# Performance work log

Measured on AMD Instinct MI355X. Metric: run time of the kernel, lower is better.

Reference implementation:

```python
import jax, jax.numpy as jnp
import numpy as np

B, H, L, D = 8, 8, 2048, 512

def setup_inputs() -> dict:
    key = jax.random.key(0)
    k1, k2 = jax.random.split(key)
    x = jax.random.normal(k1, (B, H, L, D), dtype=jnp.float32)
    mask = jnp.ones((B, L), dtype=jnp.int32)  # unused by the layer's call()
    complex_weight = 0.02 * jax.random.normal(k2, (H, L, D, 2), dtype=jnp.float32)
    return {"x": x, "mask": mask, "complex_weight": complex_weight}

def reference(x, mask, complex_weight):
    # FFT over the innermost (model_size) axis, matching tf.signal.fft
    fft_x = jnp.fft.fft(x.astype(jnp.complex64), axis=-1)
    w = jax.lax.complex(complex_weight[..., 0], complex_weight[..., 1])  # (H, L, D)
    gated = w * fft_x  # broadcast over batch
    out = jnp.fft.ifft(gated, axis=-1).real.astype(jnp.float32)
    return out
```

## Files before the change

kernel.cpp:

```cpp
#include <hip/hip_runtime.h>
#include <math.h>


#define HL 16384

__device__ __forceinline__ float2 cadd(float2 a, float2 b){ return make_float2(a.x+b.x, a.y+b.y); }
__device__ __forceinline__ float2 csub(float2 a, float2 b){ return make_float2(a.x-b.x, a.y-b.y); }
__device__ __forceinline__ float2 cmul(float2 a, float2 b){ return make_float2(a.x*b.x - a.y*b.y, a.x*b.y + a.y*b.x); }

__device__ __forceinline__ float2 twiddle(float f) {
    return make_float2(__builtin_amdgcn_cosf(f), -__builtin_amdgcn_sinf(f));
}

__device__ __forceinline__ void lds_order() {
    __builtin_amdgcn_wave_barrier();
}

__device__ __forceinline__ void fft8(float2 x[8]) {
    const float c = 0.70710678118654752f;
    float2 u0 = cadd(x[0], x[4]);
    float2 u1 = cadd(x[1], x[5]);
    float2 u2 = cadd(x[2], x[6]);
    float2 u3 = cadd(x[3], x[7]);
    float2 v0 = csub(x[0], x[4]);
    float2 t1 = csub(x[1], x[5]);
    float2 t2 = csub(x[2], x[6]);
    float2 t3 = csub(x[3], x[7]);
    float2 v1 = make_float2(c*(t1.x + t1.y), c*(t1.y - t1.x));
    float2 v2 = make_float2(t2.y, -t2.x);
    float2 v3 = make_float2(c*(t3.y - t3.x), -c*(t3.x + t3.y));
    float2 p0 = cadd(u0, u2), p1 = cadd(u1, u3);
    float2 q0 = csub(u0, u2), q1t = csub(u1, u3);
    float2 q1 = make_float2(q1t.y, -q1t.x);
    x[0] = cadd(p0, p1);
    x[4] = csub(p0, p1);
    x[2] = cadd(q0, q1);
    x[6] = csub(q0, q1);
    float2 r0 = cadd(v0, v2), r1 = cadd(v1, v3);
    float2 s0 = csub(v0, v2), s1t = csub(v1, v3);
    float2 s1 = make_float2(s1t.y, -s1t.x);
    x[1] = cadd(r0, r1);
    x[5] = csub(r0, r1);
    x[3] = cadd(s0, s1);
    x[7] = csub(s0, s1);
}

__device__ __forceinline__ void fft512_t(float2 v[8], int role, int lane, float2* sc,
                                         const float2* __restrict__ twA,
                                         const float2 tw2[8])
{
    fft8(v);
    #pragma unroll
    for (int k = 1; k < 8; ++k) v[k] = cmul(v[k], twA[role*7 + (k-1)]);
    lds_order();
    #pragma unroll
    for (int k1 = 0; k1 < 8; ++k1) sc[k1*72 + role] = v[k1];
    lds_order();
    const int k1 = lane >> 3, m2 = lane & 7;
    float2 u[8];
    #pragma unroll
    for (int m1 = 0; m1 < 8; ++m1) u[m1] = sc[k1*72 + 8*m1 + m2];
    fft8(u);
    #pragma unroll
    for (int j = 1; j < 8; ++j) u[j] = cmul(u[j], tw2[j]);
    lds_order();
    #pragma unroll
    for (int j1 = 0; j1 < 8; ++j1) sc[k1*72 + 9*j1 + m2] = u[j1];
    lds_order();
    const int j1 = lane & 7;
    #pragma unroll
    for (int m = 0; m < 8; ++m) v[m] = sc[k1*72 + 9*j1 + m];
    fft8(v);
}

__global__ __launch_bounds__(256, 8) void sgn_fft_nof(
    const float* __restrict__ x,
    const float* __restrict__ cw,
    float* __restrict__ out)
{
    __shared__ __align__(16) float2 sc[4][8*72];
    __shared__ __align__(16) float2 twA[64*7];

    const int tid  = threadIdx.x;
    const int wid  = tid >> 6;
    const int lane = tid & 63;
    const int dsl  = ((lane & 7) << 3) | (lane >> 3);
    const int hl   = blockIdx.x;

    {
        const int role = tid & 63, j = tid >> 6;
        twA[role*7 + 2*j] = twiddle((float)(role*(2*j+1)) * (1.0f/512.0f));
        if (j < 3)
            twA[role*7 + 2*j + 1] = twiddle((float)(role*(2*j+2)) * (1.0f/512.0f));
    }

    float2 tw2[8];
    {
        const int m2 = lane & 7;
        tw2[1] = twiddle((float)m2 * (1.0f/64.0f));
        tw2[2] = cmul(tw2[1], tw2[1]);
        tw2[3] = cmul(tw2[1], tw2[2]);
        tw2[4] = cmul(tw2[2], tw2[2]);
        tw2[5] = cmul(tw2[1], tw2[4]);
        tw2[6] = cmul(tw2[2], tw2[4]);
        tw2[7] = cmul(tw2[3], tw2[4]);
    }
    __syncthreads();

    const int r1 = (wid       * HL + hl) * 512;
    const int r2 = ((wid + 4) * HL + hl) * 512;
    const float2* __restrict__ cw2 = (const float2*)cw;
    const int wrow = hl * 512;
    float2* scw = &sc[wid][0];

    float2 v[8];
    #pragma unroll
    for (int j = 0; j < 8; ++j) {
        v[j].x = x[r1 + 64*j + lane];
        v[j].y = x[r2 + 64*j + lane];
    }

    fft512_t(v, lane, lane, scw, twA, tw2);

    const float hs = 0.5f / 512.0f;
    #pragma unroll
    for (int j2 = 0; j2 < 8; ++j2) {
        const int k  = dsl + 64*j2;
        const int nk = (512 - k) & 511;
        const float2 wk  = cw2[wrow + k];
        const float2 wnk = cw2[wrow + nk];
        const float2 wp  = make_float2(hs*(wk.x + wnk.x), hs*(wk.y - wnk.y));
        const float2 g   = cmul(wp, v[j2]);
        v[j2] = make_float2(g.x, -g.y);
    }

    fft512_t(v, dsl, lane, scw, twA, tw2);

    #pragma unroll
    for (int j2 = 0; j2 < 8; ++j2) {
        const int k = dsl + 64*j2;
        out[r1 + k] =  v[j2].x;
        out[r2 + k] = -v[j2].y;
    }
}

extern "C" void kernel_launch(void* const* d_in, const int* in_sizes, int n_in,
                              void* d_out, int out_size, void* d_ws, size_t ws_size,
                              hipStream_t stream) {
    const float* x  = (const float*)d_in[0];
    const float* cw = (const float*)d_in[2];
    float* out = (float*)d_out;

    sgn_fft_nof<<<dim3(HL), dim3(256), 0, stream>>>(x, cw, out);
}
```

Baseline: 483.2 us.

## Vectorize global loads/stores via LDS staging and async-load weights into LDS

New measurement: 473.8 us. About the same (-1.9%).

```diff
diff --git a/kernel.cpp b/kernel.cpp
--- a/kernel.cpp
+++ b/kernel.cpp
@@ -73,12 +73,16 @@
     fft8(v);
 }
 
-__global__ __launch_bounds__(256, 8) void sgn_fft_nof(
+using gu32 = __attribute__((address_space(1))) const unsigned int;
+using lu32 = __attribute__((address_space(3))) unsigned int;
+
+__global__ __launch_bounds__(256, 4) void sgn_fft_vec(
     const float* __restrict__ x,
     const float* __restrict__ cw,
     float* __restrict__ out)
 {
     __shared__ __align__(16) float2 sc[4][8*72];
+    __shared__ __align__(16) float  cwb[4][1024];
     __shared__ __align__(16) float2 twA[64*7];
 
     const int tid  = threadIdx.x;
@@ -87,13 +91,29 @@
     const int dsl  = ((lane & 7) << 3) | (lane >> 3);
     const int hl   = blockIdx.x;
 
+    const int r1 = (wid       * HL + hl) * 512;
+    const int r2 = ((wid + 4) * HL + hl) * 512;
+
+    {
+        const float* cwrow = cw + (size_t)hl * 1024;
+        #pragma unroll
+        for (int c = 0; c < 4; ++c) {
+            __builtin_amdgcn_global_load_lds((gu32*)(cwrow + c*256 + lane*4),
+                                             (lu32*)(&cwb[wid][c*256]), 16, 0, 0);
+        }
+    }
+
+    const float4 a0 = *(const float4*)(x + r1 + 4*lane);
+    const float4 a1 = *(const float4*)(x + r1 + 4*lane + 256);
+    const float4 b0 = *(const float4*)(x + r2 + 4*lane);
+    const float4 b1 = *(const float4*)(x + r2 + 4*lane + 256);
+
     {
         const int role = tid & 63, j = tid >> 6;
         twA[role*7 + 2*j] = twiddle((float)(role*(2*j+1)) * (1.0f/512.0f));
         if (j < 3)
             twA[role*7 + 2*j + 1] = twiddle((float)(role*(2*j+2)) * (1.0f/512.0f));
     }
-
     float2 tw2[8];
     {
         const int m2 = lane & 7;
@@ -107,40 +127,56 @@
     }
     __syncthreads();
 
-    const int r1 = (wid       * HL + hl) * 512;
-    const int r2 = ((wid + 4) * HL + hl) * 512;
-    const float2* __restrict__ cw2 = (const float2*)cw;
-    const int wrow = hl * 512;
     float2* scw = &sc[wid][0];
 
+    {
+        float2* AB = scw;
+        *(float4*)&AB[      4*lane    ] = make_float4(a0.x, b0.x, a0.y, b0.y);
+        *(float4*)&AB[      4*lane + 2] = make_float4(a0.z, b0.z, a0.w, b0.w);
+        *(float4*)&AB[256 + 4*lane    ] = make_float4(a1.x, b1.x, a1.y, b1.y);
+        *(float4*)&AB[256 + 4*lane + 2] = make_float4(a1.z, b1.z, a1.w, b1.w);
+    }
+    lds_order();
     float2 v[8];
     #pragma unroll
-    for (int j = 0; j < 8; ++j) {
-        v[j].x = x[r1 + 64*j + lane];
-        v[j].y = x[r2 + 64*j + lane];
-    }
+    for (int j = 0; j < 8; ++j) v[j] = scw[64*j + lane];
+    lds_order();
 
     fft512_t(v, lane, lane, scw, twA, tw2);
 
-    const float hs = 0.5f / 512.0f;
-    #pragma unroll
-    for (int j2 = 0; j2 < 8; ++j2) {
-        const int k  = dsl + 64*j2;
-        const int nk = (512 - k) & 511;
-        const float2 wk  = cw2[wrow + k];
-        const float2 wnk = cw2[wrow + nk];
-        const float2 wp  = make_float2(hs*(wk.x + wnk.x), hs*(wk.y - wnk.y));
-        const float2 g   = cmul(wp, v[j2]);
-        v[j2] = make_float2(g.x, -g.y);
+    asm volatile("s_waitcnt vmcnt(0)" ::: "memory");
+    {
+        const float2* __restrict__ cwf = (const float2*)&cwb[wid][0];
+        const float hs = 0.5f / 512.0f;
+        #pragma unroll
+        for (int j2 = 0; j2 < 8; ++j2) {
+            const int k  = dsl + 64*j2;
+            const int nk = (512 - k) & 511;
+            const float2 wk  = cwf[k];
+            const float2 wnk = cwf[nk];
+            const float2 wp  = make_float2(hs*(wk.x + wnk.x), hs*(wk.y - wnk.y));
+            const float2 g   = cmul(wp, v[j2]);
+            v[j2] = make_float2(g.x, -g.y);
+        }
     }
 
     fft512_t(v, dsl, lane, scw, twA, tw2);
 
+    lds_order();
+    {
+        float2* OD = scw;
+        #pragma unroll
+        for (int j2 = 0; j2 < 8; ++j2)
+            OD[dsl + 64*j2] = make_float2(v[j2].x, -v[j2].y);
+    }
+    lds_order();
     #pragma unroll
-    for (int j2 = 0; j2 < 8; ++j2) {
-        const int k = dsl + 64*j2;
-        out[r1 + k] =  v[j2].x;
-        out[r2 + k] = -v[j2].y;
+    for (int c = 0; c < 2; ++c) {
+        const float2* OD = scw;
+        const float4 p = *(const float4*)&OD[4*lane + 256*c];
+        const float4 q = *(const float4*)&OD[4*lane + 256*c + 2];
+        *(float4*)(out + r1 + 4*lane + 256*c) = make_float4(p.x, p.z, q.x, q.z);
+        *(float4*)(out + r2 + 4*lane + 256*c) = make_float4(p.y, p.w, q.y, q.w);
     }
 }
 
@@ -151,5 +187,5 @@
     const float* cw = (const float*)d_in[2];
     float* out = (float*)d_out;
 
-    sgn_fft_nof<<<dim3(HL), dim3(256), 0, stream>>>(x, cw, out);
+    sgn_fft_vec<<<dim3(HL), dim3(256), 0, stream>>>(x, cw, out);
 }
```
